# Kernel optimization log

Hardware: AMD Instinct MI355X
Metric: run time of the kernel (lower is better)

Reference implementation:

```python
import jax, jax.numpy as jnp
import numpy as np

N = 50000        # nodes
E = 800000       # edges
D_IN = 64        # input_dim
D_E = 16         # edge_dim
D_OUT = 64       # output_dim
HEADS = 8
HEAD_DIM = D_OUT // HEADS
COMB = 2 * D_IN + D_E  # 144


def _linear_init(key, fan_in, fan_out):
    kw, kb = jax.random.split(key)
    lim = 1.0 / np.sqrt(fan_in)
    W = jax.random.uniform(kw, (fan_in, fan_out), minval=-lim, maxval=lim, dtype=jnp.float32)
    b = jax.random.uniform(kb, (fan_out,), minval=-lim, maxval=lim, dtype=jnp.float32)
    return W, b


def setup_inputs() -> dict:
    key = jax.random.key(0)
    ks = jax.random.split(key, 16)
    inp = {
        "x": jax.random.normal(ks[0], (N, D_IN), dtype=jnp.float32),
        "edge_attr": jax.random.normal(ks[1], (E, D_E), dtype=jnp.float32),
        "edge_index": jax.random.randint(ks[2], (2, E), 0, N, dtype=jnp.int32),
        "q": jax.random.uniform(ks[3], (1, D_OUT), dtype=jnp.float32) * 0.1,
    }
    # three ResidualStacks: k (COMB->D_OUT), v (COMB->D_OUT), out (D_OUT->D_OUT)
    for pre, fan_in, kbase in (("k", COMB, 4), ("v", COMB, 8), ("o", D_OUT, 12)):
        W0, b0 = _linear_init(ks[kbase], fan_in, D_OUT)
        W1, b1 = _linear_init(ks[kbase + 1], D_OUT, D_OUT)
        W2, b2 = _linear_init(ks[kbase + 2], D_OUT, D_OUT)
        inp.update({f"{pre}_W0": W0, f"{pre}_b0": b0,
                    f"{pre}_W1": W1, f"{pre}_b1": b1,
                    f"{pre}_W2": W2, f"{pre}_b2": b2})
    return inp


def residual_stack(h, W0, b0, W1, b1, W2, b2, last_activation):
    # input projection + ReLU, then 2 residual linear blocks
    h = jax.nn.relu(h @ W0 + b0)
    h = jax.nn.relu(h + h @ W1 + b1)
    h = h + h @ W2 + b2
    if last_activation:
        h = jax.nn.relu(h)
    return h


def neighborhood_attention(q, k, v, index):
    # q: (1, D_OUT), k/v: (E, D_OUT), index: (E,) destination node ids
    kh = k.reshape(E, HEADS, HEAD_DIM)
    qh = q.reshape(1, HEADS, HEAD_DIM)
    scores = jnp.sum(qh * kh, axis=-1) / np.sqrt(HEAD_DIM)  # (E, HEADS)
    m = jax.ops.segment_max(scores, index, num_segments=N)  # (N, HEADS)
    ex = jnp.exp(scores - jax.lax.stop_gradient(m)[index])
    denom = jax.ops.segment_sum(ex, index, num_segments=N)  # (N, HEADS)
    alpha = ex / denom[index]
    vh = v.reshape(E, HEADS, HEAD_DIM)
    return (alpha[:, :, None] * vh).reshape(E, D_OUT)


def reference(x, edge_attr, edge_index, q,
              k_W0, k_b0, k_W1, k_b1, k_W2, k_b2,
              v_W0, v_b0, v_W1, v_b1, v_W2, v_b2,
              o_W0, o_b0, o_W1, o_b1, o_W2, o_b2):
    src, dst = edge_index[0], edge_index[1]
    feat = jnp.concatenate([x[src], x[dst], edge_attr], axis=-1)  # (E, COMB)
    k = residual_stack(feat, k_W0, k_b0, k_W1, k_b1, k_W2, k_b2, last_activation=False)
    v = residual_stack(feat, v_W0, v_b0, v_W1, v_b1, v_W2, v_b2, last_activation=False)
    messages = neighborhood_attention(q, k, v, dst)               # (E, D_OUT)
    aggr = jax.ops.segment_sum(messages, dst, num_segments=N)    # (N, D_OUT)
    out = residual_stack(jax.nn.relu(aggr), o_W0, o_b0, o_W1, o_b1, o_W2, o_b2, last_activation=False)
    # skip_connection=True, input_dim == output_dim -> identity skip
    return jax.nn.relu(x + out)
```

## Files before the change

### kernel.cpp

```cpp
#include <hip/hip_runtime.h>

#define N_NODES 50000
#define E_EDGES 800000
#define D_OUT   64
#define COMB    144

typedef float  f32x4  __attribute__((ext_vector_type(4)));
typedef __bf16 bf16x8 __attribute__((ext_vector_type(8)));
typedef __bf16 bf16x4 __attribute__((ext_vector_type(4)));

#define WS_DEG     0
#define WS_START   200704
#define WS_CURSOR  401408
#define WS_WTS     602112
#define WS_PERM    709888
#define WS_MSG     3909888

#define BIG_ELEMS    (64*168)
#define SMALL_ELEMS  (64*72)

__global__ __launch_bounds__(256) void prep_kernel(
    const float* __restrict__ kW0, const float* __restrict__ kW1, const float* __restrict__ kW2,
    const float* __restrict__ vW0, const float* __restrict__ vW1, const float* __restrict__ vW2,
    const float* __restrict__ oW0, const float* __restrict__ oW1, const float* __restrict__ oW2,
    __bf16* __restrict__ wout)
{
    const int b = blockIdx.x, tid = threadIdx.x;
    const float* src;
    __bf16* dst;
    int K, Kpad, lb;
    if (b < 42)      { src = kW0; dst = wout;             K = 144; Kpad = 168; lb = b; }
    else if (b < 84) { src = vW0; dst = wout + BIG_ELEMS; K = 144; Kpad = 168; lb = b - 42; }
    else {
        const int id = (b - 84) / 18; lb = (b - 84) % 18;
        const float* s7[7] = {kW1, kW2, vW1, vW2, oW0, oW1, oW2};
        src = s7[id]; dst = wout + 2 * BIG_ELEMS + id * SMALL_ELEMS;
        K = 64; Kpad = 72;
    }
    const int idx = lb * 256 + tid;
    const int col = idx / Kpad, k = idx % Kpad;
    dst[idx] = (k < K) ? (__bf16)src[k * 64 + col] : (__bf16)0.f;
}

__global__ __launch_bounds__(256) void deg_kernel(const int* __restrict__ edge_index,
                                                  int* __restrict__ deg)
{
    const int e = blockIdx.x * 256 + threadIdx.x;
    if (e < E_EDGES) atomicAdd(&deg[edge_index[E_EDGES + e]], 1);
}

__global__ __launch_bounds__(1024) void scan_kernel(const int* __restrict__ deg,
                                                    int* __restrict__ start,
                                                    int* __restrict__ cursor)
{
    __shared__ int wsum[16];
    __shared__ int carry_s;
    const int tid = threadIdx.x, lane = tid & 63, wv = tid >> 6;
    if (tid == 0) carry_s = 0;
    __syncthreads();
    for (int base = 0; base < N_NODES; base += 1024) {
        const int i = base + tid;
        const int v = (i < N_NODES) ? deg[i] : 0;
        int sc = v;
        #pragma unroll
        for (int off = 1; off < 64; off <<= 1) {
            int t = __shfl_up(sc, off);
            if (lane >= off) sc += t;
        }
        if (lane == 63) wsum[wv] = sc;
        const int c = carry_s;
        __syncthreads();
        if (wv == 0 && lane < 16) {
            int ws = wsum[lane];
            #pragma unroll
            for (int off = 1; off < 16; off <<= 1) {
                int t = __shfl_up(ws, off);
                if (lane >= off) ws += t;
            }
            wsum[lane] = ws;
        }
        __syncthreads();
        const int woff = (wv == 0) ? 0 : wsum[wv - 1];
        const int excl = c + woff + sc - v;
        if (i < N_NODES) { start[i] = excl; cursor[i] = excl; }
        __syncthreads();
        if (tid == 0) carry_s = c + wsum[15];
        __syncthreads();
    }
}

__global__ __launch_bounds__(256) void perm_kernel(const int* __restrict__ edge_index,
                                                   int* __restrict__ cursor,
                                                   int* __restrict__ perm)
{
    const int e = blockIdx.x * 256 + threadIdx.x;
    if (e < E_EDGES) {
        const int d = edge_index[E_EDGES + e];
        perm[atomicAdd(&cursor[d], 1)] = e;
    }
}

__device__ __forceinline__ void gemm64(const __bf16* Arow, const __bf16* Wt,
                                       int hi, int row16, f32x4 acc[4])
{
    #pragma unroll
    for (int kc = 0; kc < 2; ++kc) {
        const bf16x8 a = *(const bf16x8*)(Arow + kc * 32 + hi * 8);
        #pragma unroll
        for (int n = 0; n < 4; ++n) {
            const bf16x8 bfr = *(const bf16x8*)(Wt + (n * 16 + row16) * 72 + kc * 32 + hi * 8);
            acc[n] = __builtin_amdgcn_mfma_f32_16x16x32_bf16(a, bfr, acc[n], 0, 0, 0);
        }
    }
}

__device__ __forceinline__ bf16x8 pack8(float4 a, float4 b) {
    bf16x8 r;
    r[0] = (__bf16)a.x; r[1] = (__bf16)a.y; r[2] = (__bf16)a.z; r[3] = (__bf16)a.w;
    r[4] = (__bf16)b.x; r[5] = (__bf16)b.y; r[6] = (__bf16)b.z; r[7] = (__bf16)b.w;
    return r;
}

__global__ __launch_bounds__(256, 6) void edge_kernel(
    const float* __restrict__ x,
    const float* __restrict__ edge_attr,
    const int*   __restrict__ edge_index,
    const float* __restrict__ q,
    const float* __restrict__ kb0, const float* __restrict__ kb1, const float* __restrict__ kb2,
    const float* __restrict__ vb0, const float* __restrict__ vb1, const float* __restrict__ vb2,
    const __bf16* __restrict__ kW0t, const __bf16* __restrict__ kW1t, const __bf16* __restrict__ kW2t,
    const __bf16* __restrict__ vW0t, const __bf16* __restrict__ vW1t, const __bf16* __restrict__ vW2t,
    __bf16* __restrict__ msg)
{
    __shared__ __bf16 H_s[64][72];

    const int tid   = threadIdx.x;
    const int lane  = tid & 63;
    const int w     = tid >> 6;
    const int row16 = lane & 15;
    const int hi    = lane >> 4;
    const int wrow  = w * 16;

    const int e0 = (blockIdx.x * 4 + w) * 16;
    const int er = e0 + row16;

    const int src  = edge_index[er];
    const int dstn = edge_index[E_EDGES + er];

    bf16x8 af[5];
    {
        const float* xs = &x[(size_t)src * 64 + hi * 8];
        af[0] = pack8(*(const float4*)xs,        *(const float4*)(xs + 4));
        af[1] = pack8(*(const float4*)(xs + 32), *(const float4*)(xs + 36));
        const float* xd = &x[(size_t)dstn * 64 + hi * 8];
        af[2] = pack8(*(const float4*)xd,        *(const float4*)(xd + 4));
        af[3] = pack8(*(const float4*)(xd + 32), *(const float4*)(xd + 36));
        if (hi < 2) {
            const float* ep = &edge_attr[(size_t)er * 16 + hi * 8];
            af[4] = pack8(*(const float4*)ep, *(const float4*)(ep + 4));
        } else {
            #pragma unroll
            for (int i = 0; i < 8; ++i) af[4][i] = (__bf16)0.f;
        }
    }

    const __bf16* hrow = &H_s[wrow + row16][0];
    float ex[4][4];

    {
        f32x4 acc[4] = {{0,0,0,0},{0,0,0,0},{0,0,0,0},{0,0,0,0}};
        #pragma unroll
        for (int kc = 0; kc < 5; ++kc) {
            #pragma unroll
            for (int n = 0; n < 4; ++n) {
                const bf16x8 bfr = *(const bf16x8*)(kW0t + (n * 16 + row16) * 168 + kc * 32 + hi * 8);
                acc[n] = __builtin_amdgcn_mfma_f32_16x16x32_bf16(af[kc], bfr, acc[n], 0, 0, 0);
            }
        }
        float h0[4][4];
        #pragma unroll
        for (int n = 0; n < 4; ++n) {
            const float bias = kb0[n * 16 + row16];
            #pragma unroll
            for (int r = 0; r < 4; ++r) {
                h0[n][r] = fmaxf(acc[n][r] + bias, 0.f);
                H_s[wrow + hi * 4 + r][n * 16 + row16] = (__bf16)h0[n][r];
            }
        }
        __builtin_amdgcn_wave_barrier();

        f32x4 acc1[4] = {{0,0,0,0},{0,0,0,0},{0,0,0,0},{0,0,0,0}};
        gemm64(hrow, kW1t, hi, row16, acc1);
        float h1[4][4];
        #pragma unroll
        for (int n = 0; n < 4; ++n) {
            const float bias = kb1[n * 16 + row16];
            #pragma unroll
            for (int r = 0; r < 4; ++r) {
                h1[n][r] = fmaxf(h0[n][r] + acc1[n][r] + bias, 0.f);
                H_s[wrow + hi * 4 + r][n * 16 + row16] = (__bf16)h1[n][r];
            }
        }
        __builtin_amdgcn_wave_barrier();

        f32x4 acc2[4] = {{0,0,0,0},{0,0,0,0},{0,0,0,0},{0,0,0,0}};
        gemm64(hrow, kW2t, hi, row16, acc2);

        #pragma unroll
        for (int n = 0; n < 4; ++n) {
            const float bias = kb2[n * 16 + row16];
            const float qv   = q[n * 16 + row16];
            #pragma unroll
            for (int r = 0; r < 4; ++r) {
                const float kk = h1[n][r] + acc2[n][r] + bias;
                float p2 = qv * kk;
                p2 += __shfl_xor(p2, 1);
                p2 += __shfl_xor(p2, 2);
                p2 += __shfl_xor(p2, 4);
                ex[n][r] = __expf(p2 * 0.35355339059327373f);
            }
        }
    }

    float vv[4][4];
    {
        f32x4 acc[4] = {{0,0,0,0},{0,0,0,0},{0,0,0,0},{0,0,0,0}};
        #pragma unroll
        for (int kc = 0; kc < 5; ++kc) {
            #pragma unroll
            for (int n = 0; n < 4; ++n) {
                const bf16x8 bfr = *(const bf16x8*)(vW0t + (n * 16 + row16) * 168 + kc * 32 + hi * 8);
                acc[n] = __builtin_amdgcn_mfma_f32_16x16x32_bf16(af[kc], bfr, acc[n], 0, 0, 0);
            }
        }
        float h0[4][4];
        #pragma unroll
        for (int n = 0; n < 4; ++n) {
            const float bias = vb0[n * 16 + row16];
            #pragma unroll
            for (int r = 0; r < 4; ++r) {
                h0[n][r] = fmaxf(acc[n][r] + bias, 0.f);
                H_s[wrow + hi * 4 + r][n * 16 + row16] = (__bf16)h0[n][r];
            }
        }
        __builtin_amdgcn_wave_barrier();

        f32x4 acc1[4] = {{0,0,0,0},{0,0,0,0},{0,0,0,0},{0,0,0,0}};
        gemm64(hrow, vW1t, hi, row16, acc1);
        float h1[4][4];
        #pragma unroll
        for (int n = 0; n < 4; ++n) {
            const float bias = vb1[n * 16 + row16];
            #pragma unroll
            for (int r = 0; r < 4; ++r) {
                h1[n][r] = fmaxf(h0[n][r] + acc1[n][r] + bias, 0.f);
                H_s[wrow + hi * 4 + r][n * 16 + row16] = (__bf16)h1[n][r];
            }
        }
        __builtin_amdgcn_wave_barrier();

        f32x4 acc2[4] = {{0,0,0,0},{0,0,0,0},{0,0,0,0},{0,0,0,0}};
        gemm64(hrow, vW2t, hi, row16, acc2);
        #pragma unroll
        for (int n = 0; n < 4; ++n) {
            const float bias = vb2[n * 16 + row16];
            #pragma unroll
            for (int r = 0; r < 4; ++r)
                vv[n][r] = h1[n][r] + acc2[n][r] + bias;
        }
    }

    #pragma unroll
    for (int r = 0; r < 4; ++r) {
        __bf16* mrow = msg + (size_t)(e0 + hi * 4 + r) * 72;
        #pragma unroll
        for (int n = 0; n < 4; ++n)
            mrow[n * 16 + row16] = (__bf16)(ex[n][r] * vv[n][r]);
        if ((row16 & 7) == 0) {
            #pragma unroll
            for (int n = 0; n < 4; ++n)
                mrow[64 + 2 * n + (row16 >> 3)] = (__bf16)ex[n][r];
        }
    }
}

__global__ __launch_bounds__(256, 8) void aggr_kernel(
    const int* __restrict__ start, const int* __restrict__ endc,
    const int* __restrict__ perm, const __bf16* __restrict__ msg,
    float* __restrict__ aggr_out)
{
    const int lane = threadIdx.x & 63;
    const int n    = blockIdx.x * 4 + (threadIdx.x >> 6);
    if (n >= N_NODES) return;
    int s = start[n];
    const int e = endc[n];
    float accm = 0.f, acce = 0.f;
    for (; s + 1 < e; s += 2) {
        const int p0 = perm[s], p1 = perm[s + 1];
        const size_t b0 = (size_t)p0 * 72, b1 = (size_t)p1 * 72;
        const float m0 = (float)msg[b0 + lane];
        const float e0 = (float)msg[b0 + 64 + (lane >> 3)];
        const float m1 = (float)msg[b1 + lane];
        const float e1 = (float)msg[b1 + 64 + (lane >> 3)];
        accm += m0 + m1; acce += e0 + e1;
    }
    if (s < e) {
        const size_t b0 = (size_t)perm[s] * 72;
        accm += (float)msg[b0 + lane];
        acce += (float)msg[b0 + 64 + (lane >> 3)];
    }
    const float a = (acce > 0.f) ? fmaxf(accm / acce, 0.f) : 0.f;
    aggr_out[(size_t)n * 64 + lane] = a;
}

__global__ __launch_bounds__(256) void node_kernel(
    const float* __restrict__ x, const float* __restrict__ aggr_in,
    const float* __restrict__ ob0, const float* __restrict__ ob1, const float* __restrict__ ob2,
    const __bf16* __restrict__ oW0t, const __bf16* __restrict__ oW1t, const __bf16* __restrict__ oW2t,
    float* __restrict__ out)
{
    __shared__ __bf16 A_s[64][72];
    __shared__ __bf16 H_s[64][72];

    const int tid  = threadIdx.x;
    const int lane = tid & 63;
    const int w    = tid >> 6;
    const int n0   = blockIdx.x * 64;
    const int row16 = lane & 15;
    const int hi    = lane >> 4;

    {
        const int r = tid >> 2, seg = tid & 3;
        const int node = n0 + r;
        #pragma unroll
        for (int g = 0; g < 4; ++g) {
            bf16x4 h; h[0] = h[1] = h[2] = h[3] = (__bf16)0.f;
            if (node < N_NODES) {
                const float4 f = *(const float4*)&aggr_in[(size_t)node * 64 + seg * 16 + g * 4];
                h[0] = (__bf16)f.x; h[1] = (__bf16)f.y; h[2] = (__bf16)f.z; h[3] = (__bf16)f.w;
            }
            *(bf16x4*)&A_s[r][seg * 16 + g * 4] = h;
        }
    }
    __syncthreads();

    const __bf16* arow = &A_s[w * 16 + row16][0];
    const __bf16* hrow = &H_s[w * 16 + row16][0];

    f32x4 acc[4] = {{0,0,0,0},{0,0,0,0},{0,0,0,0},{0,0,0,0}};
    gemm64(arow, oW0t, hi, row16, acc);
    float h0[4][4];
    #pragma unroll
    for (int n = 0; n < 4; ++n) {
        const float bias = ob0[n * 16 + row16];
        #pragma unroll
        for (int r = 0; r < 4; ++r) {
            h0[n][r] = fmaxf(acc[n][r] + bias, 0.f);
            H_s[w * 16 + hi * 4 + r][n * 16 + row16] = (__bf16)h0[n][r];
        }
    }
    __builtin_amdgcn_wave_barrier();

    f32x4 acc1[4] = {{0,0,0,0},{0,0,0,0},{0,0,0,0},{0,0,0,0}};
    gemm64(hrow, oW1t, hi, row16, acc1);
    float h1[4][4];
    #pragma unroll
    for (int n = 0; n < 4; ++n) {
        const float bias = ob1[n * 16 + row16];
        #pragma unroll
        for (int r = 0; r < 4; ++r) {
            h1[n][r] = fmaxf(h0[n][r] + acc1[n][r] + bias, 0.f);
            H_s[w * 16 + hi * 4 + r][n * 16 + row16] = (__bf16)h1[n][r];
        }
    }
    __builtin_amdgcn_wave_barrier();

    f32x4 acc2[4] = {{0,0,0,0},{0,0,0,0},{0,0,0,0},{0,0,0,0}};
    gemm64(hrow, oW2t, hi, row16, acc2);
    #pragma unroll
    for (int n = 0; n < 4; ++n) {
        const float bias = ob2[n * 16 + row16];
        #pragma unroll
        for (int r = 0; r < 4; ++r) {
            const int node = n0 + w * 16 + hi * 4 + r;
            if (node < N_NODES) {
                const int col = n * 16 + row16;
                const float o = h1[n][r] + acc2[n][r] + bias;
                out[(size_t)node * 64 + col] = fmaxf(x[(size_t)node * 64 + col] + o, 0.f);
            }
        }
    }
}

extern "C" void kernel_launch(void* const* d_in, const int* in_sizes, int n_in,
                              void* d_out, int out_size, void* d_ws, size_t ws_size,
                              hipStream_t stream) {
    const float* x  = (const float*)d_in[0];
    const float* ea = (const float*)d_in[1];
    const int*   ei = (const int*)d_in[2];
    const float* q  = (const float*)d_in[3];
    const float* kW0 = (const float*)d_in[4];  const float* kb0 = (const float*)d_in[5];
    const float* kW1 = (const float*)d_in[6];  const float* kb1 = (const float*)d_in[7];
    const float* kW2 = (const float*)d_in[8];  const float* kb2 = (const float*)d_in[9];
    const float* vW0 = (const float*)d_in[10]; const float* vb0 = (const float*)d_in[11];
    const float* vW1 = (const float*)d_in[12]; const float* vb1 = (const float*)d_in[13];
    const float* vW2 = (const float*)d_in[14]; const float* vb2 = (const float*)d_in[15];
    const float* oW0 = (const float*)d_in[16]; const float* ob0 = (const float*)d_in[17];
    const float* oW1 = (const float*)d_in[18]; const float* ob1 = (const float*)d_in[19];
    const float* oW2 = (const float*)d_in[20]; const float* ob2 = (const float*)d_in[21];

    char* ws = (char*)d_ws;
    int*    deg    = (int*)(ws + WS_DEG);
    int*    start  = (int*)(ws + WS_START);
    int*    cursor = (int*)(ws + WS_CURSOR);
    __bf16* wts    = (__bf16*)(ws + WS_WTS);
    int*    perm   = (int*)(ws + WS_PERM);
    __bf16* msg    = (__bf16*)(ws + WS_MSG);
    float*  aggrf  = (float*)d_out;

    __bf16* kW0t = wts;
    __bf16* vW0t = wts + BIG_ELEMS;
    __bf16* sm   = wts + 2 * BIG_ELEMS;
    __bf16* kW1t = sm;                   __bf16* kW2t = sm + SMALL_ELEMS;
    __bf16* vW1t = sm + 2 * SMALL_ELEMS; __bf16* vW2t = sm + 3 * SMALL_ELEMS;
    __bf16* oW0t = sm + 4 * SMALL_ELEMS; __bf16* oW1t = sm + 5 * SMALL_ELEMS;
    __bf16* oW2t = sm + 6 * SMALL_ELEMS;

    hipMemsetAsync(deg, 0, (size_t)N_NODES * sizeof(int), stream);

    deg_kernel<<<E_EDGES / 256, 256, 0, stream>>>(ei, deg);
    scan_kernel<<<1, 1024, 0, stream>>>(deg, start, cursor);
    perm_kernel<<<E_EDGES / 256, 256, 0, stream>>>(ei, cursor, perm);

    prep_kernel<<<210, 256, 0, stream>>>(kW0, kW1, kW2, vW0, vW1, vW2, oW0, oW1, oW2, wts);

    edge_kernel<<<E_EDGES / 64, 256, 0, stream>>>(
        x, ea, ei, q,
        kb0, kb1, kb2, vb0, vb1, vb2,
        kW0t, kW1t, kW2t, vW0t, vW1t, vW2t,
        msg);

    aggr_kernel<<<(N_NODES + 3) / 4, 256, 0, stream>>>(start, cursor, perm, msg, aggrf);

    node_kernel<<<(N_NODES + 63) / 64, 256, 0, stream>>>(
        x, aggrf, ob0, ob1, ob2, oW0t, oW1t, oW2t, (float*)d_out);
}
```

Measured before the change: 523.1 us.

## Split message buffer into aligned value and exp arrays, vectorize aggregation

The 72-wide interleaved bf16 message buffer becomes a 64-wide value array plus a separate 8-wide exp-sum array, so each row is 128-byte aligned. The edge kernel writes both with nontemporal stores and its occupancy hint rises from 6 to 8 waves. The aggregation kernel now has four lane groups each handle every fourth edge with 8-byte vector loads, then combines them with cross-lane shuffles. This cuts per-edge load instructions and unaligned row access, at the cost of a shuffle reduction, possible register pressure from the tighter launch bound, and one extra workspace region.

```diff
diff --git a/kernel.cpp b/kernel.cpp
--- a/kernel.cpp
+++ b/kernel.cpp
@@ -10,11 +10,12 @@
 typedef __bf16 bf16x4 __attribute__((ext_vector_type(4)));
 
 #define WS_DEG     0
-#define WS_START   200704
-#define WS_CURSOR  401408
-#define WS_WTS     602112
-#define WS_PERM    709888
-#define WS_MSG     3909888
+#define WS_START   200064
+#define WS_CURSOR  400128
+#define WS_WTS     600192
+#define WS_PERM    707840
+#define WS_VMSG    3907840
+#define WS_EXMSG   106307840
 
 #define BIG_ELEMS    (64*168)
 #define SMALL_ELEMS  (64*72)
@@ -121,7 +122,14 @@
     return r;
 }
 
-__global__ __launch_bounds__(256, 6) void edge_kernel(
+__device__ __forceinline__ void nt_store_bf16(__bf16* p, float v) {
+    __bf16 b = (__bf16)v;
+    short s;
+    __builtin_memcpy(&s, &b, 2);
+    __builtin_nontemporal_store(s, reinterpret_cast<short*>(p));
+}
+
+__global__ __launch_bounds__(256, 8) void edge_kernel(
     const float* __restrict__ x,
     const float* __restrict__ edge_attr,
     const int*   __restrict__ edge_index,
@@ -130,7 +138,7 @@
     const float* __restrict__ vb0, const float* __restrict__ vb1, const float* __restrict__ vb2,
     const __bf16* __restrict__ kW0t, const __bf16* __restrict__ kW1t, const __bf16* __restrict__ kW2t,
     const __bf16* __restrict__ vW0t, const __bf16* __restrict__ vW1t, const __bf16* __restrict__ vW2t,
-    __bf16* __restrict__ msg)
+    __bf16* __restrict__ vmsg, __bf16* __restrict__ exmsg)
 {
     __shared__ __bf16 H_s[64][72];
 
@@ -272,45 +280,55 @@
 
     #pragma unroll
     for (int r = 0; r < 4; ++r) {
-        __bf16* mrow = msg + (size_t)(e0 + hi * 4 + r) * 72;
+        const int erow = e0 + hi * 4 + r;
+        __bf16* mrow = vmsg + (size_t)erow * 64;
         #pragma unroll
         for (int n = 0; n < 4; ++n)
-            mrow[n * 16 + row16] = (__bf16)(ex[n][r] * vv[n][r]);
+            nt_store_bf16(mrow + n * 16 + row16, ex[n][r] * vv[n][r]);
         if ((row16 & 7) == 0) {
+            __bf16* erow8 = exmsg + (size_t)erow * 8;
             #pragma unroll
             for (int n = 0; n < 4; ++n)
-                mrow[64 + 2 * n + (row16 >> 3)] = (__bf16)ex[n][r];
+                nt_store_bf16(erow8 + 2 * n + (row16 >> 3), ex[n][r]);
         }
     }
 }
 
 __global__ __launch_bounds__(256, 8) void aggr_kernel(
     const int* __restrict__ start, const int* __restrict__ endc,
-    const int* __restrict__ perm, const __bf16* __restrict__ msg,
+    const int* __restrict__ perm,
+    const __bf16* __restrict__ vmsg, const __bf16* __restrict__ exmsg,
     float* __restrict__ aggr_out)
 {
     const int lane = threadIdx.x & 63;
     const int n    = blockIdx.x * 4 + (threadIdx.x >> 6);
     if (n >= N_NODES) return;
-    int s = start[n];
-    const int e = endc[n];
-    float accm = 0.f, acce = 0.f;
-    for (; s + 1 < e; s += 2) {
-        const int p0 = perm[s], p1 = perm[s + 1];
-        const size_t b0 = (size_t)p0 * 72, b1 = (size_t)p1 * 72;
-        const float m0 = (float)msg[b0 + lane];
-        const float e0 = (float)msg[b0 + 64 + (lane >> 3)];
-        const float m1 = (float)msg[b1 + lane];
-        const float e1 = (float)msg[b1 + 64 + (lane >> 3)];
-        accm += m0 + m1; acce += e0 + e1;
-    }
-    if (s < e) {
-        const size_t b0 = (size_t)perm[s] * 72;
-        accm += (float)msg[b0 + lane];
-        acce += (float)msg[b0 + 64 + (lane >> 3)];
-    }
-    const float a = (acce > 0.f) ? fmaxf(accm / acce, 0.f) : 0.f;
-    aggr_out[(size_t)n * 64 + lane] = a;
+    const int g = lane >> 4;
+    const int l = lane & 15;
+    const int s0 = start[n], e1 = endc[n];
+
+    float m0 = 0.f, m1 = 0.f, m2 = 0.f, m3 = 0.f, ae = 0.f;
+    for (int i = s0 + g; i < e1; i += 4) {
+        const int pe = perm[i];
+        const bf16x4 v = *(const bf16x4*)&vmsg[(size_t)pe * 64 + l * 4];
+        ae += (float)exmsg[(size_t)pe * 8 + (l >> 1)];
+        m0 += (float)v[0]; m1 += (float)v[1]; m2 += (float)v[2]; m3 += (float)v[3];
+    }
+    #pragma unroll
+    for (int m = 16; m < 64; m <<= 1) {
+        m0 += __shfl_xor(m0, m); m1 += __shfl_xor(m1, m);
+        m2 += __shfl_xor(m2, m); m3 += __shfl_xor(m3, m);
+        ae += __shfl_xor(ae, m);
+    }
+    if (g == 0) {
+        const float inv = (ae > 0.f) ? 1.f / ae : 0.f;
+        float4 o;
+        o.x = fmaxf(m0 * inv, 0.f);
+        o.y = fmaxf(m1 * inv, 0.f);
+        o.z = fmaxf(m2 * inv, 0.f);
+        o.w = fmaxf(m3 * inv, 0.f);
+        *(float4*)&aggr_out[(size_t)n * 64 + l * 4] = o;
+    }
 }
 
 __global__ __launch_bounds__(256) void node_kernel(
@@ -333,13 +351,13 @@
         const int r = tid >> 2, seg = tid & 3;
         const int node = n0 + r;
         #pragma unroll
-        for (int g = 0; g < 4; ++g) {
+        for (int gg = 0; gg < 4; ++gg) {
             bf16x4 h; h[0] = h[1] = h[2] = h[3] = (__bf16)0.f;
             if (node < N_NODES) {
-                const float4 f = *(const float4*)&aggr_in[(size_t)node * 64 + seg * 16 + g * 4];
+                const float4 f = *(const float4*)&aggr_in[(size_t)node * 64 + seg * 16 + gg * 4];
                 h[0] = (__bf16)f.x; h[1] = (__bf16)f.y; h[2] = (__bf16)f.z; h[3] = (__bf16)f.w;
             }
-            *(bf16x4*)&A_s[r][seg * 16 + g * 4] = h;
+            *(bf16x4*)&A_s[r][seg * 16 + gg * 4] = h;
         }
     }
     __syncthreads();
@@ -415,7 +433,8 @@
     int*    cursor = (int*)(ws + WS_CURSOR);
     __bf16* wts    = (__bf16*)(ws + WS_WTS);
     int*    perm   = (int*)(ws + WS_PERM);
-    __bf16* msg    = (__bf16*)(ws + WS_MSG);
+    __bf16* vmsg   = (__bf16*)(ws + WS_VMSG);
+    __bf16* exmsg  = (__bf16*)(ws + WS_EXMSG);
     float*  aggrf  = (float*)d_out;
 
     __bf16* kW0t = wts;
@@ -438,9 +457,9 @@
         x, ea, ei, q,
         kb0, kb1, kb2, vb0, vb1, vb2,
         kW0t, kW1t, kW2t, vW0t, vW1t, vW2t,
-        msg);
-
-    aggr_kernel<<<(N_NODES + 3) / 4, 256, 0, stream>>>(start, cursor, perm, msg, aggrf);
+        vmsg, exmsg);
+
+    aggr_kernel<<<(N_NODES + 3) / 4, 256, 0, stream>>>(start, cursor, perm, vmsg, exmsg, aggrf);
 
     node_kernel<<<(N_NODES + 63) / 64, 256, 0, stream>>>(
         x, aggrf, ob0, ob1, ob2, oW0t, oW1t, oW2t, (float*)d_out);
```

Result: slower. 627.7 us (+20.0%).
